# Performance work log

Measured on AMD Instinct MI355X. Metric: run time of the kernel, lower is better.

Reference implementation:

```python
import jax, jax.numpy as jnp
import numpy as np
from jax import lax

B, T, D, H = 128, 512, 512, 512
FORGET_BIAS = 1.0  # TF BasicLSTMCell default


def setup_inputs() -> dict:
    key = jax.random.key(0)
    k1, k2, k3 = jax.random.split(key, 3)
    scale = 1.0 / np.sqrt(D + H)
    return {
        "word_vectors": jax.random.normal(k1, (B, T, D), dtype=jnp.float32),
        "num_words": jax.random.randint(k2, (B,), 0, T, dtype=jnp.int32),
        "init_c": jnp.zeros((B, H), dtype=jnp.float32),
        "init_h": jnp.zeros((B, H), dtype=jnp.float32),
        "W": jax.random.normal(k3, (D + H, 4 * H), dtype=jnp.float32) * scale,  # gates i,j,f,o
        "b": jnp.zeros((4 * H,), dtype=jnp.float32),
    }


def reference(word_vectors, num_words, init_c, init_h, W, b):
    # word_vectors: [B, T, D] -> time-major [T, B, D]
    xs = jnp.transpose(word_vectors, (1, 0, 2))
    ts = jnp.arange(T, dtype=num_words.dtype)

    def step(carry, inp):
        c, h = carry
        x, t = inp
        z = jnp.concatenate([x, h], axis=-1) @ W + b  # [B, 4H]
        i, j, f, o = jnp.split(z, 4, axis=-1)  # TF gate order
        new_c = c * jax.nn.sigmoid(f + FORGET_BIAS) + jax.nn.sigmoid(i) * jnp.tanh(j)
        new_h = jnp.tanh(new_c) * jax.nn.sigmoid(o)
        mask = (t < num_words)[:, None]  # [B, 1]
        # static_rnn sequence_length semantics: copy state through, zero outputs
        c2 = jnp.where(mask, new_c, c)
        h2 = jnp.where(mask, new_h, h)
        out = jnp.where(mask, new_h, jnp.zeros_like(new_h))
        return (c2, h2), out

    (final_c, final_h), outputs = lax.scan(step, (init_c, init_h), (xs, ts))
    # outputs: [T, B, H] (time-major, like the list returned by static_rnn)
    return outputs, final_c, final_h
```

## Files before the change

### kernel.cpp

```cpp
#include <hip/hip_runtime.h>


#define B_ 128
#define T_ 512
#define D_ 512
#define H_ 512

typedef __bf16 bf16x8 __attribute__((ext_vector_type(8)));
typedef float f32x4 __attribute__((ext_vector_type(4)));
typedef unsigned long long u64;

static __device__ __forceinline__ unsigned short f2bf(float f) {
  return __builtin_bit_cast(unsigned short, (__bf16)f);
}
static __device__ __forceinline__ float fast_sigmoid(float x) {
  return __builtin_amdgcn_rcpf(1.f + __expf(-x));
}
static __device__ __forceinline__ float fast_tanh(float x) {
  float xc = fminf(fmaxf(x, -15.f), 15.f);
  float t = __expf(-2.f * xc);
  return (1.f - t) * __builtin_amdgcn_rcpf(1.f + t);
}

__global__ __launch_bounds__(256) void pack_w_kernel(const float* __restrict__ W,
                                                     unsigned short* __restrict__ Wp) {
  int tid = blockIdx.x * 256 + threadIdx.x;
  int j = tid & 7;
  int lane = (tid >> 3) & 63;
  int f = tid >> 9;
  int kt = f & 31;
  int w = (f >> 5) & 7;
  int hb = f >> 8;
  int k = (kt << 5) + ((lane >> 4) << 3) + j;
  int col = ((w & 3) << 9) + (hb << 5) + ((w >> 2) << 4) + (lane & 15);
  Wp[tid] = f2bf(W[k * 2048 + col]);
}

__global__ void init_bar_kernel(int* __restrict__ bar) {
  bar[blockIdx.x * 256 + threadIdx.x] = 0;
}

__global__ __launch_bounds__(512, 2) void lstm_persistent(
    const float* __restrict__ wv, const int* __restrict__ nw,
    const float* __restrict__ ic, const float* __restrict__ ih,
    const float* __restrict__ bias, const unsigned short* __restrict__ Wp,
    unsigned int* __restrict__ hg, int* __restrict__ bar,
    float* __restrict__ out) {
  __shared__ __align__(16) unsigned short hlds[16 * 512];
  __shared__ __align__(16) unsigned short xlds[2][16 * 512];
  __shared__ float zbuf[8][16][17];

  const int tid = threadIdx.x;
  const int wgid = blockIdx.x;
  const int mg = wgid & 7;
  const int hb = wgid >> 3;
  const int w = tid >> 6;
  const int lane = tid & 63;
  const int g = w & 3;
  const int jj = w >> 2;

  const int er = tid >> 5;
  const int ec = tid & 31;
  const int grow = (mg << 4) + er;
  const int gcol = (hb << 5) + ec;

  const int nwv = nw[grow];
  float c_reg = ic[grow * H_ + gcol];
  float h_reg = ih[grow * H_ + gcol];

  uint4 wfrag[32];
  {
    const uint4* wp = (const uint4*)Wp + (size_t)((hb * 8 + w) * 32) * 64 + lane;
#pragma unroll
    for (int kt = 0; kt < 32; ++kt) wfrag[kt] = wp[kt * 64];
  }
  const float bv = bias[(g << 9) + (hb << 5) + (jj << 4) + (lane & 15)];

  int* gflags = bar + (mg << 8);
  int* myflag = gflags + hb * 16;
  int* fq0 = gflags + ((2 * w) << 4);
  int* fq1 = gflags + ((2 * w + 1) << 4);

  const int hslot = (hb << 9) + ((er | ((ec >> 3) << 4)) << 3) + (ec & 7);
  unsigned int* hg0 = hg + mg * 4096;
  unsigned int* hg1 = hg + (8 + mg) * 4096;

  auto publish_h = [&](unsigned int* dst) {
    unsigned int hv = (unsigned int)f2bf(h_reg);
    unsigned int up = (unsigned int)__shfl_down((int)hv, 1);
    if ((tid & 1) == 0)
      __hip_atomic_store(dst + (hslot >> 1), hv | (up << 16), __ATOMIC_RELAXED,
                         __HIP_MEMORY_SCOPE_AGENT);
  };

  auto arrive = [&](int epoch) {
    if (tid == 0)
      __hip_atomic_store(myflag, epoch, __ATOMIC_RELAXED, __HIP_MEMORY_SCOPE_AGENT);
  };

  auto wait_stage = [&](int epoch, const unsigned int* src) {
    while (true) {
      int a = __hip_atomic_load(fq0, __ATOMIC_RELAXED, __HIP_MEMORY_SCOPE_AGENT);
      int b = __hip_atomic_load(fq1, __ATOMIC_RELAXED, __HIP_MEMORY_SCOPE_AGENT);
      if (a >= epoch && b >= epoch) break;
      __builtin_amdgcn_s_sleep(1);
    }
    __asm__ volatile("" ::: "memory");
    const u64* s = (const u64*)src;
    u64* d = (u64*)hlds;
    u64 tmp[8];
#pragma unroll
    for (int q = 0; q < 2; ++q)
#pragma unroll
      for (int i = 0; i < 4; ++i)
        tmp[q * 4 + i] = __hip_atomic_load(s + ((2 * w + q) << 8) + (i << 6) + lane,
                                           __ATOMIC_RELAXED, __HIP_MEMORY_SCOPE_AGENT);
#pragma unroll
    for (int q = 0; q < 2; ++q)
#pragma unroll
      for (int i = 0; i < 4; ++i)
        d[((2 * w + q) << 8) + (i << 6) + lane] = tmp[q * 4 + i];
  };

  auto load_x = [&](int buf, int tt) {
    if (tt >= T_) return;
#pragma unroll
    for (int s = 0; s < 2; ++s) {
      int e = tid + (s << 9);
      int ktx = e >> 6;
      int le = e & 63;
      int r = le & 15;
      int d = (ktx << 5) + ((le >> 4) << 3);
      const float* src = wv + ((size_t)((mg << 4) + r) * T_ + tt) * D_ + d;
      float4 xa = *(const float4*)src;
      float4 xb = *(const float4*)(src + 4);
      bf16x8 v;
      v[0] = (__bf16)xa.x; v[1] = (__bf16)xa.y; v[2] = (__bf16)xa.z; v[3] = (__bf16)xa.w;
      v[4] = (__bf16)xb.x; v[5] = (__bf16)xb.y; v[6] = (__bf16)xb.z; v[7] = (__bf16)xb.w;
      *(bf16x8*)&xlds[buf][(ktx << 9) + (le << 3)] = v;
    }
  };

  auto xpart = [&](int buf) {
    f32x4 a = {0.f, 0.f, 0.f, 0.f};
#pragma unroll
    for (int kt = 0; kt < 16; ++kt) {
      bf16x8 af = *(const bf16x8*)&xlds[buf][(kt << 9) + (lane << 3)];
      a = __builtin_amdgcn_mfma_f32_16x16x32_bf16(
          af, __builtin_bit_cast(bf16x8, wfrag[kt]), a, 0, 0, 0);
    }
    return a;
  };

  load_x(0, 0);
  __syncthreads();
  f32x4 acc = xpart(0);
  load_x(1, 1);
  publish_h(hg0);
  __syncthreads();
  arrive(1);
  wait_stage(1, hg0);
  __syncthreads();

  for (int t = 0; t < T_; ++t) {
    const int par = t & 1;
    unsigned int* hdst = par ? hg0 : hg1;

    f32x4 acc2 = {0.f, 0.f, 0.f, 0.f};
#pragma unroll
    for (int kt = 0; kt < 8; ++kt) {
      bf16x8 a0 = *(const bf16x8*)&hlds[((2 * kt) << 9) + (lane << 3)];
      bf16x8 a1 = *(const bf16x8*)&hlds[((2 * kt + 1) << 9) + (lane << 3)];
      acc = __builtin_amdgcn_mfma_f32_16x16x32_bf16(
          a0, __builtin_bit_cast(bf16x8, wfrag[16 + 2 * kt]), acc, 0, 0, 0);
      acc2 = __builtin_amdgcn_mfma_f32_16x16x32_bf16(
          a1, __builtin_bit_cast(bf16x8, wfrag[17 + 2 * kt]), acc2, 0, 0, 0);
    }
    {
      int q = lane >> 4, cl = lane & 15;
#pragma unroll
      for (int v = 0; v < 4; ++v)
        zbuf[w][q * 4 + v][cl] = acc[v] + acc2[v] + bv;
    }
    __syncthreads();
    {
      int ej = ec >> 4, ecl = ec & 15;
      float zi = zbuf[ej * 4 + 0][er][ecl];
      float zj = zbuf[ej * 4 + 1][er][ecl];
      float zf = zbuf[ej * 4 + 2][er][ecl];
      float zo = zbuf[ej * 4 + 3][er][ecl];
      float si = fast_sigmoid(zi);
      float sf = fast_sigmoid(zf + 1.f);
      float so = fast_sigmoid(zo);
      float tj = fast_tanh(zj);
      float nc = c_reg * sf + si * tj;
      float nh = fast_tanh(nc) * so;
      bool m = t < nwv;
      c_reg = m ? nc : c_reg;
      h_reg = m ? nh : h_reg;
      publish_h(hdst);
      out[(size_t)t * (B_ * H_) + grow * H_ + gcol] = m ? nh : 0.f;
    }
    __syncthreads();
    arrive(t + 2);
    if (t + 1 < T_) {
      acc = xpart(1 - par);
      load_x(par, t + 2);
      wait_stage(t + 2, hdst);
    }
    __syncthreads();
  }

  size_t base = (size_t)T_ * (B_ * H_);
  out[base + grow * H_ + gcol] = c_reg;
  out[base + B_ * H_ + grow * H_ + gcol] = h_reg;
}

extern "C" void kernel_launch(void* const* d_in, const int* in_sizes, int n_in,
                              void* d_out, int out_size, void* d_ws, size_t ws_size,
                              hipStream_t stream) {
  const float* wv = (const float*)d_in[0];
  const int* nw = (const int*)d_in[1];
  const float* ic = (const float*)d_in[2];
  const float* ih = (const float*)d_in[3];
  const float* W = (const float*)d_in[4];
  const float* bias = (const float*)d_in[5];
  float* out = (float*)d_out;

  char* ws = (char*)d_ws;
  unsigned short* Wp = (unsigned short*)ws;
  unsigned int* hg = (unsigned int*)(ws + (4u << 20));
  int* bar = (int*)(ws + (4u << 20) + (256u << 10));

  init_bar_kernel<<<8, 256, 0, stream>>>(bar);
  pack_w_kernel<<<(1 << 21) / 256, 256, 0, stream>>>(W, Wp);
  lstm_persistent<<<128, 512, 0, stream>>>(wv, nw, ic, ih, bias, Wp, hg, bar, out);
}
```

Measured before the change: 1.755 ms.

## Replace flag barrier with poison-sentinel data polling over a triple-buffered h exchange

Drops the separate epoch flag array. Each workgroup now polls the hidden-state slots directly and treats data as ready once no POISON sentinel values remain, using a three-slot ring that is re-poisoned two steps later. This removes one round trip per step (flag write, flag read, then data read) from the serial recurrence. It also splits the x prefetch into an early global load and a late LDS commit, loads the initial h straight from the input, and uses lighter LDS-only barriers. The trade-off is wider polling traffic on h data, and correctness now depends on no valid bf16 pair ever equalling the sentinel and on the ordering of the re-poison stores.

```diff
diff --git a/kernel.cpp b/kernel.cpp
--- a/kernel.cpp
+++ b/kernel.cpp
@@ -5,6 +5,7 @@
 #define T_ 512
 #define D_ 512
 #define H_ 512
+#define POISON 0xFFFFFFFFu
 
 typedef __bf16 bf16x8 __attribute__((ext_vector_type(8)));
 typedef float f32x4 __attribute__((ext_vector_type(4)));
@@ -21,6 +22,16 @@
   float t = __expf(-2.f * xc);
   return (1.f - t) * __builtin_amdgcn_rcpf(1.f + t);
 }
+static __device__ __forceinline__ bool clean64(u64 v) {
+  return ((unsigned int)v != POISON) && ((unsigned int)(v >> 32) != POISON);
+}
+
+#define LBAR()                                             \
+  do {                                                     \
+    __asm__ volatile("s_waitcnt lgkmcnt(0)" ::: "memory"); \
+    __builtin_amdgcn_s_barrier();                          \
+    __asm__ volatile("" ::: "memory");                     \
+  } while (0)
 
 __global__ __launch_bounds__(256) void pack_w_kernel(const float* __restrict__ W,
                                                      unsigned short* __restrict__ Wp) {
@@ -36,16 +47,15 @@
   Wp[tid] = f2bf(W[k * 2048 + col]);
 }
 
-__global__ void init_bar_kernel(int* __restrict__ bar) {
-  bar[blockIdx.x * 256 + threadIdx.x] = 0;
+__global__ __launch_bounds__(1024) void init_poison_kernel(unsigned int* __restrict__ hg) {
+  hg[blockIdx.x * 1024 + threadIdx.x] = POISON;
 }
 
 __global__ __launch_bounds__(512, 2) void lstm_persistent(
     const float* __restrict__ wv, const int* __restrict__ nw,
     const float* __restrict__ ic, const float* __restrict__ ih,
     const float* __restrict__ bias, const unsigned short* __restrict__ Wp,
-    unsigned int* __restrict__ hg, int* __restrict__ bar,
-    float* __restrict__ out) {
+    unsigned int* __restrict__ hg, float* __restrict__ out) {
   __shared__ __align__(16) unsigned short hlds[16 * 512];
   __shared__ __align__(16) unsigned short xlds[2][16 * 512];
   __shared__ float zbuf[8][16][17];
@@ -76,14 +86,9 @@
   }
   const float bv = bias[(g << 9) + (hb << 5) + (jj << 4) + (lane & 15)];
 
-  int* gflags = bar + (mg << 8);
-  int* myflag = gflags + hb * 16;
-  int* fq0 = gflags + ((2 * w) << 4);
-  int* fq1 = gflags + ((2 * w + 1) << 4);
+  auto slotp = [&](int s) { return hg + (size_t)(s * 8 + mg) * 4096; };
 
   const int hslot = (hb << 9) + ((er | ((ec >> 3) << 4)) << 3) + (ec & 7);
-  unsigned int* hg0 = hg + mg * 4096;
-  unsigned int* hg1 = hg + (8 + mg) * 4096;
 
   auto publish_h = [&](unsigned int* dst) {
     unsigned int hv = (unsigned int)f2bf(h_reg);
@@ -93,47 +98,56 @@
                          __HIP_MEMORY_SCOPE_AGENT);
   };
 
-  auto arrive = [&](int epoch) {
-    if (tid == 0)
-      __hip_atomic_store(myflag, epoch, __ATOMIC_RELAXED, __HIP_MEMORY_SCOPE_AGENT);
-  };
-
-  auto wait_stage = [&](int epoch, const unsigned int* src) {
+  auto wait_stage = [&](const unsigned int* slot) {
+    const u64* s = (const u64*)slot;
+    const u64* cs0 = s + ((2 * w) << 7);
+    const u64* cs1 = s + ((2 * w + 1) << 7);
+    u64 a0, a1, b0, b1;
     while (true) {
-      int a = __hip_atomic_load(fq0, __ATOMIC_RELAXED, __HIP_MEMORY_SCOPE_AGENT);
-      int b = __hip_atomic_load(fq1, __ATOMIC_RELAXED, __HIP_MEMORY_SCOPE_AGENT);
-      if (a >= epoch && b >= epoch) break;
+      a0 = __hip_atomic_load(cs0 + lane, __ATOMIC_RELAXED, __HIP_MEMORY_SCOPE_AGENT);
+      a1 = __hip_atomic_load(cs0 + 64 + lane, __ATOMIC_RELAXED, __HIP_MEMORY_SCOPE_AGENT);
+      b0 = __hip_atomic_load(cs1 + lane, __ATOMIC_RELAXED, __HIP_MEMORY_SCOPE_AGENT);
+      b1 = __hip_atomic_load(cs1 + 64 + lane, __ATOMIC_RELAXED, __HIP_MEMORY_SCOPE_AGENT);
+      bool ok = clean64(a0) && clean64(a1) && clean64(b0) && clean64(b1);
+      if (__all(ok)) break;
       __builtin_amdgcn_s_sleep(1);
     }
-    __asm__ volatile("" ::: "memory");
-    const u64* s = (const u64*)src;
     u64* d = (u64*)hlds;
-    u64 tmp[8];
-#pragma unroll
-    for (int q = 0; q < 2; ++q)
-#pragma unroll
-      for (int i = 0; i < 4; ++i)
-        tmp[q * 4 + i] = __hip_atomic_load(s + ((2 * w + q) << 8) + (i << 6) + lane,
-                                           __ATOMIC_RELAXED, __HIP_MEMORY_SCOPE_AGENT);
-#pragma unroll
-    for (int q = 0; q < 2; ++q)
-#pragma unroll
-      for (int i = 0; i < 4; ++i)
-        d[((2 * w + q) << 8) + (i << 6) + lane] = tmp[q * 4 + i];
-  };
-
-  auto load_x = [&](int buf, int tt) {
+    d[((2 * w) << 7) + lane] = a0;
+    d[((2 * w) << 7) + 64 + lane] = a1;
+    d[((2 * w + 1) << 7) + lane] = b0;
+    d[((2 * w + 1) << 7) + 64 + lane] = b1;
+  };
+
+  auto repoison = [&](unsigned int* slot) {
+    if (tid < 256)
+      __hip_atomic_store(slot + (hb << 8) + tid, POISON, __ATOMIC_RELAXED,
+                         __HIP_MEMORY_SCOPE_AGENT);
+  };
+
+  float4 xr[4];
+  auto xissue = [&](int tt) {
     if (tt >= T_) return;
 #pragma unroll
-    for (int s = 0; s < 2; ++s) {
-      int e = tid + (s << 9);
+    for (int s2 = 0; s2 < 2; ++s2) {
+      int e = tid + (s2 << 9);
       int ktx = e >> 6;
       int le = e & 63;
       int r = le & 15;
       int d = (ktx << 5) + ((le >> 4) << 3);
       const float* src = wv + ((size_t)((mg << 4) + r) * T_ + tt) * D_ + d;
-      float4 xa = *(const float4*)src;
-      float4 xb = *(const float4*)(src + 4);
+      xr[2 * s2] = *(const float4*)src;
+      xr[2 * s2 + 1] = *(const float4*)(src + 4);
+    }
+  };
+  auto xcommit = [&](int buf, int tt) {
+    if (tt >= T_) return;
+#pragma unroll
+    for (int s2 = 0; s2 < 2; ++s2) {
+      int e = tid + (s2 << 9);
+      int ktx = e >> 6;
+      int le = e & 63;
+      float4 xa = xr[2 * s2], xb = xr[2 * s2 + 1];
       bf16x8 v;
       v[0] = (__bf16)xa.x; v[1] = (__bf16)xa.y; v[2] = (__bf16)xa.z; v[3] = (__bf16)xa.w;
       v[4] = (__bf16)xb.x; v[5] = (__bf16)xb.y; v[6] = (__bf16)xb.z; v[7] = (__bf16)xb.w;
@@ -152,19 +166,31 @@
     return a;
   };
 
-  load_x(0, 0);
+  xissue(0); xcommit(0, 0);
+  xissue(1); xcommit(1, 1);
+#pragma unroll
+  for (int s2 = 0; s2 < 2; ++s2) {
+    int e = tid + (s2 << 9);
+    int ktx = e >> 6;
+    int le = e & 63;
+    int r = le & 15;
+    int d = (ktx << 5) + ((le >> 4) << 3);
+    const float* src = ih + (size_t)((mg << 4) + r) * H_ + d;
+    float4 ha = *(const float4*)src;
+    float4 hbv = *(const float4*)(src + 4);
+    bf16x8 v;
+    v[0] = (__bf16)ha.x; v[1] = (__bf16)ha.y; v[2] = (__bf16)ha.z; v[3] = (__bf16)ha.w;
+    v[4] = (__bf16)hbv.x; v[5] = (__bf16)hbv.y; v[6] = (__bf16)hbv.z; v[7] = (__bf16)hbv.w;
+    *(bf16x8*)&hlds[(ktx << 9) + (le << 3)] = v;
+  }
   __syncthreads();
   f32x4 acc = xpart(0);
-  load_x(1, 1);
-  publish_h(hg0);
-  __syncthreads();
-  arrive(1);
-  wait_stage(1, hg0);
-  __syncthreads();
 
   for (int t = 0; t < T_; ++t) {
     const int par = t & 1;
-    unsigned int* hdst = par ? hg0 : hg1;
+    unsigned int* hdst = slotp((t + 1) % 3);
+
+    xissue(t + 2);
 
     f32x4 acc2 = {0.f, 0.f, 0.f, 0.f};
 #pragma unroll
@@ -182,7 +208,7 @@
       for (int v = 0; v < 4; ++v)
         zbuf[w][q * 4 + v][cl] = acc[v] + acc2[v] + bv;
     }
-    __syncthreads();
+    LBAR();
     {
       int ej = ec >> 4, ecl = ec & 15;
       float zi = zbuf[ej * 4 + 0][er][ecl];
@@ -201,12 +227,13 @@
       publish_h(hdst);
       out[(size_t)t * (B_ * H_) + grow * H_ + gcol] = m ? nh : 0.f;
     }
-    __syncthreads();
-    arrive(t + 2);
+    LBAR();
+
     if (t + 1 < T_) {
       acc = xpart(1 - par);
-      load_x(par, t + 2);
-      wait_stage(t + 2, hdst);
+      wait_stage(hdst);
+      repoison(slotp(t % 3));
+      xcommit(par, t + 2);
     }
     __syncthreads();
   }
@@ -230,9 +257,8 @@
   char* ws = (char*)d_ws;
   unsigned short* Wp = (unsigned short*)ws;
   unsigned int* hg = (unsigned int*)(ws + (4u << 20));
-  int* bar = (int*)(ws + (4u << 20) + (256u << 10));
-
-  init_bar_kernel<<<8, 256, 0, stream>>>(bar);
+
+  init_poison_kernel<<<96, 1024, 0, stream>>>(hg);
   pack_w_kernel<<<(1 << 21) / 256, 256, 0, stream>>>(W, Wp);
-  lstm_persistent<<<128, 512, 0, stream>>>(wv, nw, ic, ih, bias, Wp, hg, bar, out);
-}
+  lstm_persistent<<<128, 512, 0, stream>>>(wv, nw, ic, ih, bias, Wp, hg, out);
+}
```

Result: faster. 1.655 ms (-5.7%).
